# Performance work log

Measured on AMD Instinct MI355X. Metric: run time of the kernel, lower is better.

## Reference

```python
import jax, jax.numpy as jnp
import numpy as np

B, S, H = 1, 2048, 2048
NH = 16
HS = H // NH  # 128
NEG = -65504.0  # fp16 min used as additive mask value


def setup_inputs() -> dict:
    key = jax.random.key(0)
    k1, k2, k3, k4, k5 = jax.random.split(key, 5)
    hidden_states = jax.random.normal(k1, (B, S, H), dtype=jnp.float32)
    # causal left-to-right mask: 1 where attention allowed
    ltor_mask = jnp.tril(jnp.ones((S, S), dtype=jnp.float32))[None, None, :, :]
    W_qkv = jax.random.normal(k2, (H, 3 * H), dtype=jnp.float32) * (1.0 / np.sqrt(H))
    b_qkv = jax.random.normal(k3, (3 * H,), dtype=jnp.float32) * 0.01
    W_dense = jax.random.normal(k4, (H, H), dtype=jnp.float32) * (1.0 / np.sqrt(H))
    b_dense = jax.random.normal(k5, (H,), dtype=jnp.float32) * 0.01
    return {"hidden_states": hidden_states, "ltor_mask": ltor_mask,
            "W_qkv": W_qkv, "b_qkv": b_qkv, "W_dense": W_dense, "b_dense": b_dense}


def reference(hidden_states, ltor_mask, W_qkv, b_qkv, W_dense, b_dense):
    b, s, h = hidden_states.shape
    # fused QKV projection, then split along last dim (matches split_tensor_along_last_dim)
    qkv = hidden_states @ W_qkv + b_qkv  # [b, s, 3h]
    q, k, v = jnp.split(qkv, 3, axis=-1)
    q = q.reshape(b, s, NH, HS)
    k = k.reshape(b, s, NH, HS)
    v = v.reshape(b, s, NH, HS)
    scale = 1.0 / np.sqrt(HS)  # softmax_scale=None -> 1/sqrt(headdim)
    scores = jnp.einsum('bqhd,bkhd->bhqk', q, k) * scale
    scores = scores + NEG * (1.0 - ltor_mask)  # additive mask, [b,1,s,s] broadcast over heads
    probs = jax.nn.softmax(scores, axis=-1)
    ctx = jnp.einsum('bhqk,bkhd->bqhd', probs, v).reshape(b, s, h)
    out = ctx @ W_dense + b_dense  # output_dropout is identity in eval
    return out
```

## Files before the change

### kernel.cpp

```cpp
#include <hip/hip_runtime.h>
#include <math.h>

#define S_LEN 2048
#define HDIM  2048
#define NHEAD 16
#define HSZ   128
#define H3    6144

typedef __attribute__((ext_vector_type(8))) short bf16x8;
typedef __attribute__((ext_vector_type(4))) float f32x4;

__device__ inline ushort f2bf(float f) {
    union { float f; unsigned u; } c; c.f = f;
    unsigned u = c.u;
    return (ushort)((u + 0x7fffu + ((u >> 16) & 1u)) >> 16);
}
__device__ inline ushort f2bf_trunc(float f) {
    union { float f; unsigned u; } c; c.f = f;
    return (ushort)(c.u >> 16);
}

__global__ __launch_bounds__(256) void prep(
    const float* __restrict__ X,    ushort* __restrict__ Xb,
    const float* __restrict__ Wqkv, ushort* __restrict__ Wqt,
    const float* __restrict__ Wd,   ushort* __restrict__ Wdt)
{
    __shared__ ushort t[64][66];
    const int bid = blockIdx.x;
    const int tid = threadIdx.x;

    if (bid < 4096) {
        int i = bid * 1024 + tid * 4;
        float4 v = *(const float4*)(X + i);
        ushort4 o;
        o.x = f2bf(v.x); o.y = f2bf(v.y); o.z = f2bf(v.z); o.w = f2bf(v.w);
        *(ushort4*)(Xb + i) = o;
        return;
    }

    const float* W; ushort* Wt; int K, N, n0, k0;
    if (bid < 7168) {
        const int b = bid - 4096;
        W = Wqkv; Wt = Wqt; K = HDIM; N = H3;
        n0 = (b % 96) * 64; k0 = (b / 96) * 64;
    } else {
        const int b = bid - 7168;
        W = Wd; Wt = Wdt; K = HDIM; N = HDIM;
        n0 = (b % 32) * 64; k0 = (b / 32) * 64;
    }
    const int tx = tid & 15;
    const int ty = tid >> 4;
    #pragma unroll
    for (int p = 0; p < 4; p++) {
        const int k = p * 16 + ty;
        float4 v = *(const float4*)(&W[(size_t)(k0 + k) * N + n0 + tx * 4]);
        t[k][tx * 4 + 0] = f2bf(v.x);
        t[k][tx * 4 + 1] = f2bf(v.y);
        t[k][tx * 4 + 2] = f2bf(v.z);
        t[k][tx * 4 + 3] = f2bf(v.w);
    }
    __syncthreads();
    #pragma unroll
    for (int p = 0; p < 4; p++) {
        const int n = p * 16 + ty;
        ushort4 o;
        o.x = t[tx * 4 + 0][n];
        o.y = t[tx * 4 + 1][n];
        o.z = t[tx * 4 + 2][n];
        o.w = t[tx * 4 + 3][n];
        *(ushort4*)(&Wt[(size_t)(n0 + n) * K + k0 + tx * 4]) = o;
    }
}

__global__ __launch_bounds__(256) void transpose_v(const ushort* __restrict__ qkvb,
                                                   ushort* __restrict__ Vtb) {
    __shared__ ushort t[64][66];
    const int s0 = blockIdx.x * 64;
    const int d0 = blockIdx.y * 64;
    const int tx = threadIdx.x & 15;
    const int ty = threadIdx.x >> 4;
    #pragma unroll
    for (int p = 0; p < 4; p++) {
        const int s = p * 16 + ty;
        ushort4 v = *(const ushort4*)(&qkvb[(size_t)(s0 + s) * H3 + 2 * HDIM + d0 + tx * 4]);
        *(ushort4*)(&t[s][tx * 4]) = v;
    }
    __syncthreads();
    #pragma unroll
    for (int p = 0; p < 4; p++) {
        const int d = p * 16 + ty;
        ushort4 o;
        o.x = t[tx * 4 + 0][d];
        o.y = t[tx * 4 + 1][d];
        o.z = t[tx * 4 + 2][d];
        o.w = t[tx * 4 + 3][d];
        *(ushort4*)(&Vtb[(size_t)(d0 + d) * S_LEN + s0 + tx * 4]) = o;
    }
}

__global__ __launch_bounds__(512, 2) void gemm_qkv_256(
    const ushort* __restrict__ A, const ushort* __restrict__ Bt,
    const float* __restrict__ bias, ushort* __restrict__ Cb,
    int M, int N, int K)
{
    __shared__ __align__(16) ushort lds[2][2 * 256 * 64];

    const int tid  = threadIdx.x;
    const int m0   = blockIdx.y * 256;
    const int n0   = blockIdx.x * 256;
    const int w    = tid >> 6;
    const int wm   = w >> 2;
    const int wn   = w & 3;
    const int lane = tid & 63;
    const int quad = lane >> 4;
    const int l16  = lane & 15;

    const int csw   = ((tid & 7) ^ ((tid >> 3) & 7)) * 8;
    const int rbase = tid >> 3;
    const int rdsw  = l16 & 7;

    f32x4 acc[8][4] = {};

    const int T = K / 64;

    auto stage = [&](int kt, int b) {
        const int k0 = kt * 64;
        #pragma unroll
        for (int r = 0; r < 4; r++) {
            const int row = r * 64 + rbase;
            const ushort* ga = A + (size_t)(m0 + row) * K + k0 + csw;
            __builtin_amdgcn_global_load_lds(
                (const __attribute__((address_space(1))) void*)ga,
                (__attribute__((address_space(3))) void*)(&lds[b][0] + (r * 512 + tid) * 8), 16, 0, 0);
        }
        #pragma unroll
        for (int r = 0; r < 4; r++) {
            const int row = r * 64 + rbase;
            const ushort* gb = Bt + (size_t)(n0 + row) * K + k0 + csw;
            __builtin_amdgcn_global_load_lds(
                (const __attribute__((address_space(1))) void*)gb,
                (__attribute__((address_space(3))) void*)(&lds[b][16384] + (r * 512 + tid) * 8), 16, 0, 0);
        }
    };

    stage(0, 0);

    for (int t = 0; t < T; t++) {
        const int b = t & 1;
        if (t + 1 < T) {
            stage(t + 1, b ^ 1);
            asm volatile("s_waitcnt vmcnt(8)" ::: "memory");
        } else {
            asm volatile("s_waitcnt vmcnt(0)" ::: "memory");
        }
        asm volatile("s_barrier" ::: "memory");

        const ushort* bA = &lds[b][0];
        const ushort* bB = &lds[b][16384];

        bf16x8 af[4][2], bqa[2][2], bqb[2][2];

        #pragma unroll
        for (int i = 0; i < 4; i++)
            #pragma unroll
            for (int kc = 0; kc < 2; kc++)
                af[i][kc] = *(const bf16x8*)(bA + (wm * 128 + i * 16 + l16) * 64
                                               + ((((kc << 2) | quad) ^ rdsw) * 8));
        #pragma unroll
        for (int j = 0; j < 2; j++)
            #pragma unroll
            for (int kc = 0; kc < 2; kc++)
                bqa[j][kc] = *(const bf16x8*)(bB + (wn * 64 + j * 16 + l16) * 64
                                                + ((((kc << 2) | quad) ^ rdsw) * 8));
        asm volatile("s_barrier" ::: "memory");
        __builtin_amdgcn_s_setprio(1);
        #pragma unroll
        for (int i = 0; i < 4; i++)
            #pragma unroll
            for (int j = 0; j < 2; j++)
                #pragma unroll
                for (int kc = 0; kc < 2; kc++)
                    acc[i][j] = __builtin_amdgcn_mfma_f32_16x16x32_bf16(
                        af[i][kc], bqa[j][kc], acc[i][j], 0, 0, 0);
        __builtin_amdgcn_s_setprio(0);
        asm volatile("s_barrier" ::: "memory");

        #pragma unroll
        for (int j = 0; j < 2; j++)
            #pragma unroll
            for (int kc = 0; kc < 2; kc++)
                bqb[j][kc] = *(const bf16x8*)(bB + (wn * 64 + (2 + j) * 16 + l16) * 64
                                                + ((((kc << 2) | quad) ^ rdsw) * 8));
        asm volatile("s_barrier" ::: "memory");
        __builtin_amdgcn_s_setprio(1);
        #pragma unroll
        for (int i = 0; i < 4; i++)
            #pragma unroll
            for (int j = 0; j < 2; j++)
                #pragma unroll
                for (int kc = 0; kc < 2; kc++)
                    acc[i][2 + j] = __builtin_amdgcn_mfma_f32_16x16x32_bf16(
                        af[i][kc], bqb[j][kc], acc[i][2 + j], 0, 0, 0);
        __builtin_amdgcn_s_setprio(0);
        asm volatile("s_barrier" ::: "memory");

        #pragma unroll
        for (int i = 0; i < 4; i++)
            #pragma unroll
            for (int kc = 0; kc < 2; kc++)
                af[i][kc] = *(const bf16x8*)(bA + (wm * 128 + (4 + i) * 16 + l16) * 64
                                               + ((((kc << 2) | quad) ^ rdsw) * 8));
        asm volatile("s_barrier" ::: "memory");
        __builtin_amdgcn_s_setprio(1);
        #pragma unroll
        for (int i = 0; i < 4; i++)
            #pragma unroll
            for (int j = 0; j < 2; j++)
                #pragma unroll
                for (int kc = 0; kc < 2; kc++)
                    acc[4 + i][2 + j] = __builtin_amdgcn_mfma_f32_16x16x32_bf16(
                        af[i][kc], bqb[j][kc], acc[4 + i][2 + j], 0, 0, 0);
        __builtin_amdgcn_s_setprio(0);
        asm volatile("s_barrier" ::: "memory");

        __builtin_amdgcn_s_setprio(1);
        #pragma unroll
        for (int i = 0; i < 4; i++)
            #pragma unroll
            for (int j = 0; j < 2; j++)
                #pragma unroll
                for (int kc = 0; kc < 2; kc++)
                    acc[4 + i][j] = __builtin_amdgcn_mfma_f32_16x16x32_bf16(
                        af[i][kc], bqa[j][kc], acc[4 + i][j], 0, 0, 0);
        __builtin_amdgcn_s_setprio(0);
    }

    #pragma unroll
    for (int i = 0; i < 8; i++) {
        #pragma unroll
        for (int r = 0; r < 4; r++) {
            const int m = m0 + wm * 128 + i * 16 + quad * 4 + r;
            #pragma unroll
            for (int j = 0; j < 4; j++) {
                const int n = n0 + wn * 64 + j * 16 + l16;
                float v  = acc[i][j][r] + bias[n];
                float vp = __shfl_xor(v, 1, 64);
                unsigned both = (unsigned)f2bf(v) | ((unsigned)f2bf(vp) << 16);
                if ((l16 & 1) == 0)
                    *(unsigned*)(Cb + (size_t)m * N + n) = both;
            }
        }
    }
}

__global__ __launch_bounds__(256) void gemm_dense(
    const ushort* __restrict__ A, const ushort* __restrict__ Bt,
    const float* __restrict__ bias, float* __restrict__ C)
{
    __shared__ ushort sA[2 * 64 * 32];
    __shared__ ushort sB[2 * 128 * 32];

    const int tid  = threadIdx.x;
    const int m0   = blockIdx.y * 64;
    const int n0   = blockIdx.x * 128;
    const int w    = tid >> 6;
    const int lane = tid & 63;
    const int quad = lane >> 4;
    const int l16  = lane & 15;
    const int wr   = (w >> 1) * 32;
    const int wc   = (w & 1) * 64;

    f32x4 acc[2][4] = {};

    for (int k0 = 0; k0 < HDIM; k0 += 64) {
        #pragma unroll
        for (int iss = 0; iss < 2; iss++) {
            const int li  = iss * 256 + tid;
            const int c   = li >> 8;
            const int row = (li >> 2) & 63;
            const int kc  = (li & 3) * 8;
            const ushort* ga = A + (size_t)(m0 + row) * HDIM + k0 + c * 32 + kc;
            __builtin_amdgcn_global_load_lds(
                (const __attribute__((address_space(1))) void*)ga,
                (__attribute__((address_space(3))) void*)(sA + li * 8), 16, 0, 0);
        }
        #pragma unroll
        for (int iss = 0; iss < 4; iss++) {
            const int li  = iss * 256 + tid;
            const int c   = li >> 9;
            const int row = (li >> 2) & 127;
            const int kc  = (li & 3) * 8;
            const ushort* gb = Bt + (size_t)(n0 + row) * HDIM + k0 + c * 32 + kc;
            __builtin_amdgcn_global_load_lds(
                (const __attribute__((address_space(1))) void*)gb,
                (__attribute__((address_space(3))) void*)(sB + li * 8), 16, 0, 0);
        }
        __syncthreads();

        #pragma unroll
        for (int c = 0; c < 2; c++) {
            bf16x8 af[2], bq[4];
            #pragma unroll
            for (int i = 0; i < 2; i++)
                af[i] = *(const bf16x8*)(sA + c * 2048 + (wr + i * 16 + l16) * 32 + quad * 8);
            #pragma unroll
            for (int j = 0; j < 4; j++)
                bq[j] = *(const bf16x8*)(sB + c * 4096 + (wc + j * 16 + l16) * 32 + quad * 8);

            #pragma unroll
            for (int i = 0; i < 2; i++)
                #pragma unroll
                for (int j = 0; j < 4; j++)
                    acc[i][j] = __builtin_amdgcn_mfma_f32_16x16x32_bf16(
                        af[i], bq[j], acc[i][j], 0, 0, 0);
        }
        __syncthreads();
    }

    #pragma unroll
    for (int i = 0; i < 2; i++)
        #pragma unroll
        for (int r = 0; r < 4; r++) {
            const int m = m0 + wr + i * 16 + quad * 4 + r;
            #pragma unroll
            for (int j = 0; j < 4; j++) {
                const int n = n0 + wc + j * 16 + l16;
                C[(size_t)m * HDIM + n] = acc[i][j][r] + bias[n];
            }
        }
}

__global__ __launch_bounds__(256) void attn_mfma(
    const ushort* __restrict__ qkvb, const ushort* __restrict__ Vtb,
    ushort* __restrict__ ctxb)
{
    __shared__ __align__(16) ushort sK [2][64 * 128];
    __shared__ __align__(16) ushort sVt[2][128 * 64];
    __shared__ __align__(16) ushort Ps [4 * 1024];

    const int tid  = threadIdx.x;
    const int bid  = blockIdx.x;
    const int h    = bid & 15;
    const int qt   = (bid < 256) ? (31 - (bid >> 4)) : ((bid - 256) >> 4);
    const int q0   = qt * 64;
    const int w    = tid >> 6;
    const int lane = tid & 63;
    const int quad = lane >> 4;
    const int l16  = lane & 15;
    const int qr0  = q0 + w * 16;

    const float scale = 0.08838834764831845f;

    bf16x8 qf[4];
    #pragma unroll
    for (int c = 0; c < 4; c++)
        qf[c] = *(const bf16x8*)(qkvb + (size_t)(qr0 + l16) * H3 + h * HSZ + c * 32 + quad * 8);

    f32x4 o[8] = {};
    float lsum[4] = {0.f, 0.f, 0.f, 0.f};

    const int nt   = qt + 1;
    const int skey = tid >> 2;
    const int sq8  = tid & 3;

    auto stage = [&](int kt, int b) {
        const int k0 = kt * 64;
        #pragma unroll
        for (int iss = 0; iss < 4; iss++) {
            const int li = iss * 256 + tid;
            const ushort* g = qkvb + (size_t)(k0 + skey) * H3 + HDIM + h * HSZ + iss * 32 + sq8 * 8;
            __builtin_amdgcn_global_load_lds(
                (const __attribute__((address_space(1))) void*)g,
                (__attribute__((address_space(3))) void*)(&sK[b][0] + li * 8), 16, 0, 0);
        }
        #pragma unroll
        for (int iss = 0; iss < 4; iss++) {
            const int li = iss * 256 + tid;
            const int c  = li >> 9;
            const int d  = (li >> 2) & 127;
            const ushort* g = Vtb + (size_t)(h * HSZ + d) * S_LEN + k0 + c * 32 + (li & 3) * 8;
            __builtin_amdgcn_global_load_lds(
                (const __attribute__((address_space(1))) void*)g,
                (__attribute__((address_space(3))) void*)(&sVt[b][0] + li * 8), 16, 0, 0);
        }
    };

    stage(0, 0);
    const int wofs = w * 1024;

    for (int kt = 0; kt < nt; kt++) {
        const int b  = kt & 1;
        const int k0 = kt * 64;

        if (kt + 1 < nt) {
            stage(kt + 1, b ^ 1);
            asm volatile("s_waitcnt vmcnt(8)" ::: "memory");
        } else {
            asm volatile("s_waitcnt vmcnt(0)" ::: "memory");
        }
        asm volatile("s_barrier" ::: "memory");

        const ushort* bK = &sK[b][0];
        const ushort* bV = &sVt[b][0];

        f32x4 sacc[4] = {};
        #pragma unroll
        for (int jt = 0; jt < 4; jt++)
            #pragma unroll
            for (int c = 0; c < 4; c++) {
                bf16x8 kf = *(const bf16x8*)(bK + c * 2048 + (jt * 16 + l16) * 32 + quad * 8);
                sacc[jt] = __builtin_amdgcn_mfma_f32_16x16x32_bf16(qf[c], kf, sacc[jt], 0, 0, 0);
            }

        float p[4][4];
        if (kt == nt - 1) {
            #pragma unroll
            for (int jt = 0; jt < 4; jt++) {
                const int key = k0 + jt * 16 + l16;
                #pragma unroll
                for (int r = 0; r < 4; r++) {
                    float e = __expf(sacc[jt][r] * scale);
                    if (key > qr0 + quad * 4 + r) e = 0.f;
                    p[jt][r] = e;
                    lsum[r] += e;
                }
            }
        } else {
            #pragma unroll
            for (int jt = 0; jt < 4; jt++)
                #pragma unroll
                for (int r = 0; r < 4; r++) {
                    float e = __expf(sacc[jt][r] * scale);
                    p[jt][r] = e;
                    lsum[r] += e;
                }
        }

        #pragma unroll
        for (int jt = 0; jt < 4; jt++) {
            const int cpan = jt >> 1;
            const int lch  = (jt & 1) * 2 + (l16 >> 3);
            const int phys = lch ^ quad;
            #pragma unroll
            for (int r = 0; r < 4; r++) {
                const int row = quad * 4 + r;
                Ps[wofs + cpan * 512 + row * 32 + phys * 8 + (l16 & 7)] = f2bf_trunc(p[jt][r]);
            }
        }

        #pragma unroll
        for (int c = 0; c < 2; c++) {
            const int pph = quad ^ (l16 >> 2);
            bf16x8 pf = *(const bf16x8*)(Ps + wofs + c * 512 + l16 * 32 + pph * 8);
            #pragma unroll
            for (int ht = 0; ht < 8; ht++) {
                bf16x8 vf = *(const bf16x8*)(bV + c * 4096 + (ht * 16 + l16) * 32 + quad * 8);
                o[ht] = __builtin_amdgcn_mfma_f32_16x16x32_bf16(pf, vf, o[ht], 0, 0, 0);
            }
        }

        asm volatile("s_waitcnt lgkmcnt(0)" ::: "memory");
        asm volatile("s_barrier" ::: "memory");
    }

    float invl[4];
    #pragma unroll
    for (int r = 0; r < 4; r++) {
        float ls = lsum[r];
        #pragma unroll
        for (int off = 1; off < 16; off <<= 1)
            ls += __shfl_xor(ls, off, 64);
        invl[r] = 1.0f / ls;
    }
    #pragma unroll
    for (int ht = 0; ht < 8; ht++) {
        #pragma unroll
        for (int r = 0; r < 4; r++) {
            float v  = o[ht][r] * invl[r];
            float vp = __shfl_xor(v, 1, 64);
            unsigned both = (unsigned)f2bf(v) | ((unsigned)f2bf(vp) << 16);
            if ((l16 & 1) == 0)
                *(unsigned*)(ctxb + (size_t)(qr0 + quad * 4 + r) * HDIM + h * HSZ + ht * 16 + l16) = both;
        }
    }
}

extern "C" void kernel_launch(void* const* d_in, const int* in_sizes, int n_in,
                              void* d_out, int out_size, void* d_ws, size_t ws_size,
                              hipStream_t stream) {
    const float* X    = (const float*)d_in[0];
    const float* Wqkv = (const float*)d_in[2];
    const float* bqkv = (const float*)d_in[3];
    const float* Wd   = (const float*)d_in[4];
    const float* bd   = (const float*)d_in[5];
    float* out = (float*)d_out;

    ushort* Xb   = (ushort*)d_ws;
    ushort* Wqt  = Xb   + (size_t)S_LEN * HDIM;
    ushort* Wdt  = Wqt  + (size_t)H3 * HDIM;
    ushort* ctxb = Wdt  + (size_t)HDIM * HDIM;
    ushort* qkvb = ctxb + (size_t)S_LEN * HDIM;
    ushort* Vtb  = qkvb + (size_t)S_LEN * H3;

    dim3 blk(256);

    prep<<<dim3(8192), blk, 0, stream>>>(X, Xb, Wqkv, Wqt, Wd, Wdt);

    gemm_qkv_256<<<dim3(H3 / 256, S_LEN / 256), dim3(512), 0, stream>>>(
        Xb, Wqt, bqkv, qkvb, S_LEN, H3, HDIM);

    transpose_v<<<dim3(S_LEN / 64, HDIM / 64), blk, 0, stream>>>(qkvb, Vtb);

    attn_mfma<<<dim3(512), blk, 0, stream>>>(qkvb, Vtb, ctxb);

    gemm_dense<<<dim3(HDIM / 128, S_LEN / 64), blk, 0, stream>>>(
        ctxb, Wdt, bd, out);
}
```

Baseline: 287.6 us.

## Retile QKV GEMM to 256x192 blocks with split A/B staging

Changes the QKV projection GEMM block tile from 256x256 to 256x192 so the grid covers 256 blocks, matching the CU count more evenly. Warps are rearranged 4x2 with 64x96 sub-tiles, and the B tile prefetch is issued mid-iteration after the first MFMA phase instead of together with A. This targets wave-quantization tail imbalance, at the cost of a lower per-block arithmetic intensity and an extra wait/barrier per iteration.

```diff
diff --git a/kernel.cpp b/kernel.cpp
--- a/kernel.cpp
+++ b/kernel.cpp
@@ -98,58 +98,64 @@
     }
 }
 
-__global__ __launch_bounds__(512, 2) void gemm_qkv_256(
+__global__ __launch_bounds__(512, 2) void gemm_qkv_v2(
     const ushort* __restrict__ A, const ushort* __restrict__ Bt,
     const float* __restrict__ bias, ushort* __restrict__ Cb,
     int M, int N, int K)
 {
-    __shared__ __align__(16) ushort lds[2][2 * 256 * 64];
+    __shared__ __align__(16) ushort lds[2][256 * 64 + 192 * 64];
 
     const int tid  = threadIdx.x;
     const int m0   = blockIdx.y * 256;
-    const int n0   = blockIdx.x * 256;
+    const int n0   = blockIdx.x * 192;
     const int w    = tid >> 6;
-    const int wm   = w >> 2;
-    const int wn   = w & 3;
+    const int wm   = w >> 1;
+    const int wn   = w & 1;
     const int lane = tid & 63;
     const int quad = lane >> 4;
     const int l16  = lane & 15;
 
-    const int csw   = ((tid & 7) ^ ((tid >> 3) & 7)) * 8;
-    const int rbase = tid >> 3;
-    const int rdsw  = l16 & 7;
-
-    f32x4 acc[8][4] = {};
+    const int rdsw = l16 & 7;
+
+    f32x4 acc[4][6] = {};
 
     const int T = K / 64;
 
-    auto stage = [&](int kt, int b) {
+    auto stageA = [&](int kt, int b) {
         const int k0 = kt * 64;
         #pragma unroll
         for (int r = 0; r < 4; r++) {
-            const int row = r * 64 + rbase;
+            const int c    = r * 512 + tid;
+            const int row  = c >> 3;
+            const int csw  = ((c & 7) ^ (row & 7)) * 8;
             const ushort* ga = A + (size_t)(m0 + row) * K + k0 + csw;
             __builtin_amdgcn_global_load_lds(
                 (const __attribute__((address_space(1))) void*)ga,
-                (__attribute__((address_space(3))) void*)(&lds[b][0] + (r * 512 + tid) * 8), 16, 0, 0);
-        }
-        #pragma unroll
-        for (int r = 0; r < 4; r++) {
-            const int row = r * 64 + rbase;
+                (__attribute__((address_space(3))) void*)(&lds[b][0] + c * 8), 16, 0, 0);
+        }
+    };
+    auto stageB = [&](int kt, int b) {
+        const int k0 = kt * 64;
+        #pragma unroll
+        for (int r = 0; r < 3; r++) {
+            const int c    = r * 512 + tid;
+            const int row  = c >> 3;
+            const int csw  = ((c & 7) ^ (row & 7)) * 8;
             const ushort* gb = Bt + (size_t)(n0 + row) * K + k0 + csw;
             __builtin_amdgcn_global_load_lds(
                 (const __attribute__((address_space(1))) void*)gb,
-                (__attribute__((address_space(3))) void*)(&lds[b][16384] + (r * 512 + tid) * 8), 16, 0, 0);
+                (__attribute__((address_space(3))) void*)(&lds[b][16384] + c * 8), 16, 0, 0);
         }
     };
 
-    stage(0, 0);
+    stageA(0, 0);
+    stageB(0, 0);
 
     for (int t = 0; t < T; t++) {
         const int b = t & 1;
         if (t + 1 < T) {
-            stage(t + 1, b ^ 1);
-            asm volatile("s_waitcnt vmcnt(8)" ::: "memory");
+            stageA(t + 1, b ^ 1);
+            asm volatile("s_waitcnt vmcnt(4)" ::: "memory");
         } else {
             asm volatile("s_waitcnt vmcnt(0)" ::: "memory");
         }
@@ -158,26 +164,26 @@
         const ushort* bA = &lds[b][0];
         const ushort* bB = &lds[b][16384];
 
-        bf16x8 af[4][2], bqa[2][2], bqb[2][2];
+        bf16x8 af[4][2], bqa[3][2], bqb[3][2];
 
         #pragma unroll
         for (int i = 0; i < 4; i++)
             #pragma unroll
             for (int kc = 0; kc < 2; kc++)
-                af[i][kc] = *(const bf16x8*)(bA + (wm * 128 + i * 16 + l16) * 64
+                af[i][kc] = *(const bf16x8*)(bA + (wm * 64 + i * 16 + l16) * 64
                                                + ((((kc << 2) | quad) ^ rdsw) * 8));
         #pragma unroll
-        for (int j = 0; j < 2; j++)
+        for (int j = 0; j < 3; j++)
             #pragma unroll
             for (int kc = 0; kc < 2; kc++)
-                bqa[j][kc] = *(const bf16x8*)(bB + (wn * 64 + j * 16 + l16) * 64
+                bqa[j][kc] = *(const bf16x8*)(bB + (wn * 96 + j * 16 + l16) * 64
                                                 + ((((kc << 2) | quad) ^ rdsw) * 8));
         asm volatile("s_barrier" ::: "memory");
         __builtin_amdgcn_s_setprio(1);
         #pragma unroll
         for (int i = 0; i < 4; i++)
             #pragma unroll
-            for (int j = 0; j < 2; j++)
+            for (int j = 0; j < 3; j++)
                 #pragma unroll
                 for (int kc = 0; kc < 2; kc++)
                     acc[i][j] = __builtin_amdgcn_mfma_f32_16x16x32_bf16(
@@ -185,64 +191,37 @@
         __builtin_amdgcn_s_setprio(0);
         asm volatile("s_barrier" ::: "memory");
 
-        #pragma unroll
-        for (int j = 0; j < 2; j++)
+        if (t + 1 < T) stageB(t + 1, b ^ 1);
+
+        #pragma unroll
+        for (int j = 0; j < 3; j++)
             #pragma unroll
             for (int kc = 0; kc < 2; kc++)
-                bqb[j][kc] = *(const bf16x8*)(bB + (wn * 64 + (2 + j) * 16 + l16) * 64
+                bqb[j][kc] = *(const bf16x8*)(bB + (wn * 96 + (3 + j) * 16 + l16) * 64
                                                 + ((((kc << 2) | quad) ^ rdsw) * 8));
         asm volatile("s_barrier" ::: "memory");
         __builtin_amdgcn_s_setprio(1);
         #pragma unroll
         for (int i = 0; i < 4; i++)
             #pragma unroll
-            for (int j = 0; j < 2; j++)
+            for (int j = 0; j < 3; j++)
                 #pragma unroll
                 for (int kc = 0; kc < 2; kc++)
-                    acc[i][2 + j] = __builtin_amdgcn_mfma_f32_16x16x32_bf16(
-                        af[i][kc], bqb[j][kc], acc[i][2 + j], 0, 0, 0);
+                    acc[i][3 + j] = __builtin_amdgcn_mfma_f32_16x16x32_bf16(
+                        af[i][kc], bqb[j][kc], acc[i][3 + j], 0, 0, 0);
         __builtin_amdgcn_s_setprio(0);
-        asm volatile("s_barrier" ::: "memory");
-
-        #pragma unroll
-        for (int i = 0; i < 4; i++)
-            #pragma unroll
-            for (int kc = 0; kc < 2; kc++)
-                af[i][kc] = *(const bf16x8*)(bA + (wm * 128 + (4 + i) * 16 + l16) * 64
-                                               + ((((kc << 2) | quad) ^ rdsw) * 8));
-        asm volatile("s_barrier" ::: "memory");
-        __builtin_amdgcn_s_setprio(1);
-        #pragma unroll
-        for (int i = 0; i < 4; i++)
-            #pragma unroll
-            for (int j = 0; j < 2; j++)
-                #pragma unroll
-                for (int kc = 0; kc < 2; kc++)
-                    acc[4 + i][2 + j] = __builtin_amdgcn_mfma_f32_16x16x32_bf16(
-                        af[i][kc], bqb[j][kc], acc[4 + i][2 + j], 0, 0, 0);
-        __builtin_amdgcn_s_setprio(0);
-        asm volatile("s_barrier" ::: "memory");
-
-        __builtin_amdgcn_s_setprio(1);
-        #pragma unroll
-        for (int i = 0; i < 4; i++)
-            #pragma unroll
-            for (int j = 0; j < 2; j++)
-                #pragma unroll
-                for (int kc = 0; kc < 2; kc++)
-                    acc[4 + i][j] = __builtin_amdgcn_mfma_f32_16x16x32_bf16(
-                        af[i][kc], bqa[j][kc], acc[4 + i][j], 0, 0, 0);
-        __builtin_amdgcn_s_setprio(0);
-    }
-
-    #pragma unroll
-    for (int i = 0; i < 8; i++) {
+        asm volatile("s_waitcnt lgkmcnt(0)" ::: "memory");
+        asm volatile("s_barrier" ::: "memory");
+    }
+
+    #pragma unroll
+    for (int i = 0; i < 4; i++) {
         #pragma unroll
         for (int r = 0; r < 4; r++) {
-            const int m = m0 + wm * 128 + i * 16 + quad * 4 + r;
-            #pragma unroll
-            for (int j = 0; j < 4; j++) {
-                const int n = n0 + wn * 64 + j * 16 + l16;
+            const int m = m0 + wm * 64 + i * 16 + quad * 4 + r;
+            #pragma unroll
+            for (int j = 0; j < 6; j++) {
+                const int n = n0 + wn * 96 + j * 16 + l16;
                 float v  = acc[i][j][r] + bias[n];
                 float vp = __shfl_xor(v, 1, 64);
                 unsigned both = (unsigned)f2bf(v) | ((unsigned)f2bf(vp) << 16);
@@ -506,7 +485,7 @@
 
     prep<<<dim3(8192), blk, 0, stream>>>(X, Xb, Wqkv, Wqt, Wd, Wdt);
 
-    gemm_qkv_256<<<dim3(H3 / 256, S_LEN / 256), dim3(512), 0, stream>>>(
+    gemm_qkv_v2<<<dim3(H3 / 192, S_LEN / 256), dim3(512), 0, stream>>>(
         Xb, Wqt, bqkv, qkvb, S_LEN, H3, HDIM);
 
     transpose_v<<<dim3(S_LEN / 64, HDIM / 64), blk, 0, stream>>>(qkvb, Vtb);
```

Result: faster. 278.0 us (-3.3%).
